# Kernel tuning notes

Hardware: AMD Instinct MI355X
Metric: run time of the kernel (lower is better)

Reference implementation:

```python
import jax, jax.numpy as jnp
import numpy as np
import math

B, IN_CH, IMG = 32, 3, 128
D, L, H, MLP, P = 512, 8, 8, 2048, 8
HD = D // H
EPS = 1e-5


def _conv(x, w, b, stride, pad):
    y = jax.lax.conv_general_dilated(x, w, (stride, stride), pad,
                                     dimension_numbers=("NCHW", "OIHW", "NCHW"))
    return y + b[None, :, None, None]


def _gn(x, g, b, groups):
    Bn, C, Hh, W = x.shape
    xr = x.reshape(Bn, groups, C // groups, Hh, W)
    m = jnp.mean(xr, axis=(2, 3, 4), keepdims=True)
    v = jnp.var(xr, axis=(2, 3, 4), keepdims=True)
    xr = (xr - m) / jnp.sqrt(v + EPS)
    return xr.reshape(Bn, C, Hh, W) * g[None, :, None, None] + b[None, :, None, None]


def _ln(x, g, b):
    m = jnp.mean(x, axis=-1, keepdims=True)
    v = jnp.var(x, axis=-1, keepdims=True)
    return (x - m) / jnp.sqrt(v + EPS) * g + b


def _rot_half(x):
    # interleaved pairs: (x0,x1) -> (-x1,x0)
    x1, x2 = x[..., 0::2], x[..., 1::2]
    return jnp.stack((-x2, x1), axis=-1).reshape(x.shape)


def _xpos_tables(n_pos, hd):
    # faithful to rotary_embedding_torch with use_xpos=True, scale_base=512
    inv = 1.0 / (10000.0 ** (jnp.arange(0, hd, 2, dtype=jnp.float32) / hd))
    seq = jnp.arange(n_pos, dtype=jnp.float32)
    freqs = jnp.repeat(seq[:, None] * inv[None, :], 2, axis=-1)  # (n_pos, hd) interleaved
    sv = (jnp.arange(0, hd, 2, dtype=jnp.float32) + 0.4 * hd) / (1.4 * hd)
    power = (seq - n_pos // 2) / 512.0
    scale = sv[None, :] ** power[:, None]                        # (n_pos, hd//2)
    scale = jnp.concatenate([scale, scale], axis=-1)             # library uses cat, not interleave
    return jnp.cos(freqs), jnp.sin(freqs), scale


def _pos2d(N, Dd):
    g = int(math.isqrt(N))
    y = jnp.tile(jnp.arange(g), g).astype(jnp.float32)
    x = jnp.repeat(jnp.arange(g), g).astype(jnp.float32)
    dq = Dd // 4
    omega = jnp.exp(jnp.arange(dq, dtype=jnp.float32) * -(math.log(10000.0) / dq))
    px, py = x[:, None] * omega, y[:, None] * omega
    return jnp.concatenate([jnp.sin(px), jnp.cos(px), jnp.sin(py), jnp.cos(py)], axis=-1)[None]


def setup_inputs() -> dict:
    key = jax.random.key(0)
    ks = iter(jax.random.split(key, 40))
    def rn(shape, s=0.02):
        return jax.random.normal(next(ks), shape, jnp.float32) * s
    return dict(
        x=jax.random.normal(next(ks), (B, IN_CH, IMG, IMG), jnp.float32),
        conv1_w=rn((32, 3, 3, 3)), conv1_b=jnp.zeros((32,), jnp.float32),
        gn1_g=jnp.ones((32,), jnp.float32), gn1_b=jnp.zeros((32,), jnp.float32),
        conv2_w=rn((64, 32, 3, 3)), conv2_b=jnp.zeros((64,), jnp.float32),
        gn2_g=jnp.ones((64,), jnp.float32), gn2_b=jnp.zeros((64,), jnp.float32),
        patch_w=rn((D, 64, P, P)), patch_b=jnp.zeros((D,), jnp.float32),
        cls_token=rn((1, 1, D), 1.0),
        ln1_g=jnp.ones((L, D), jnp.float32), ln1_b=jnp.zeros((L, D), jnp.float32),
        qkv_w=rn((L, D, 3 * D)), qkv_b=jnp.zeros((L, 3 * D), jnp.float32),
        out_w=rn((L, D, D)), out_b=jnp.zeros((L, D), jnp.float32),
        ln2_g=jnp.ones((L, D), jnp.float32), ln2_b=jnp.zeros((L, D), jnp.float32),
        w1_w=rn((L, D, MLP)), w1_b=jnp.zeros((L, MLP), jnp.float32),
        w2_w=rn((L, D, MLP)), w2_b=jnp.zeros((L, MLP), jnp.float32),
        w3_w=rn((L, MLP, D)), w3_b=jnp.zeros((L, D), jnp.float32),
        fn_g=jnp.ones((D,), jnp.float32), fn_b=jnp.zeros((D,), jnp.float32),
    )


def _forward(x, conv1_w, conv1_b, gn1_g, gn1_b, conv2_w, conv2_b, gn2_g, gn2_b,
             patch_w, patch_b, cls_token, ln1_g, ln1_b, qkv_w, qkv_b, out_w, out_b,
             ln2_g, ln2_b, w1_w, w1_b, w2_w, w2_b, w3_w, w3_b, fn_g, fn_b):
    # conv stem (no downsample)
    f = jax.nn.gelu(_gn(_conv(x, conv1_w, conv1_b, 1, [(1, 1), (1, 1)]), gn1_g, gn1_b, 4), approximate=False)
    f = jax.nn.gelu(_gn(_conv(f, conv2_w, conv2_b, 1, [(1, 1), (1, 1)]), gn2_g, gn2_b, 8), approximate=False)
    # patch embed
    p = _conv(f, patch_w, patch_b, P, "VALID")            # (B, D, g, g)
    Bn, Dd, gh, gw = p.shape
    tokens = p.reshape(Bn, Dd, gh * gw).transpose(0, 2, 1)  # (B, N, D)
    tokens = tokens + _pos2d(gh * gw, Dd)
    xa = jnp.concatenate([jnp.broadcast_to(cls_token, (Bn, 1, Dd)), tokens], axis=1)
    # NOTE: original code applies RoPE with seq_dim=-2 on (B,S,H,hd) -> rotation indexed by HEAD axis
    cos, sin, xsc = _xpos_tables(H, HD)
    scale_att = HD ** -0.5
    for i in range(L):
        n = _ln(xa, ln1_g[i], ln1_b[i])
        qkv = (n @ qkv_w[i] + qkv_b[i]).reshape(Bn, -1, 3, H, HD)
        q, k, v = qkv[:, :, 0], qkv[:, :, 1], qkv[:, :, 2]     # (B, S, H, hd)
        q = q * cos * xsc + _rot_half(q) * sin * xsc
        k = k * cos / xsc + _rot_half(k) * sin / xsc
        attn = jax.nn.softmax(jnp.einsum("bihd,bjhd->bhij", q, k) * scale_att, axis=-1)
        y = jnp.einsum("bhij,bjhd->bihd", attn, v).reshape(Bn, -1, Dd)
        xa = xa + y @ out_w[i] + out_b[i]
        n2 = _ln(xa, ln2_g[i], ln2_b[i])
        xa = xa + (jax.nn.silu(n2 @ w1_w[i] + w1_b[i]) * (n2 @ w2_w[i] + w2_b[i])) @ w3_w[i] + w3_b[i]
    return _ln(xa, fn_g, fn_b)


def reference(x, conv1_w, conv1_b, gn1_g, gn1_b, conv2_w, conv2_b, gn2_g, gn2_b,
              patch_w, patch_b, cls_token, ln1_g, ln1_b, qkv_w, qkv_b, out_w, out_b,
              ln2_g, ln2_b, w1_w, w1_b, w2_w, w2_b, w3_w, w3_b, fn_g, fn_b):
    xa = _forward(x, conv1_w, conv1_b, gn1_g, gn1_b, conv2_w, conv2_b, gn2_g, gn2_b,
                  patch_w, patch_b, cls_token, ln1_g, ln1_b, qkv_w, qkv_b, out_w, out_b,
                  ln2_g, ln2_b, w1_w, w1_b, w2_w, w2_b, w3_w, w3_b, fn_g, fn_b)
    return (xa[:, 0], xa[:, 1:])  # (cls, patches); grid_hw is static (16,16)
```

## Files before the change

### kernel.cpp

```cpp
#include <hip/hip_runtime.h>

#define EPSV 1e-5f
typedef unsigned short u16;
typedef short bf16x8 __attribute__((ext_vector_type(8)));
typedef float f32x4 __attribute__((ext_vector_type(4)));

__device__ __forceinline__ float gelu_exact(float x) {
    return 0.5f * x * (1.0f + erff(x * 0.7071067811865475f));
}
__device__ __forceinline__ u16 to_bf(float x) {
    union { float f; unsigned u; } c; c.f = x;
    unsigned r = c.u + 0x7fffu + ((c.u >> 16) & 1u);
    return (u16)(r >> 16);
}
__device__ __forceinline__ float to_f(u16 h) {
    union { unsigned u; float f; } c; c.u = ((unsigned)h) << 16;
    return c.f;
}
__device__ __forceinline__ void gload_lds16(const void* g, void* l) {
    __builtin_amdgcn_global_load_lds((const __attribute__((address_space(1))) unsigned int*)g,
                                     (__attribute__((address_space(3))) unsigned int*)l, 16, 0, 0);
}

__global__ void k_wsfail(float* out) { out[0] = 1.0e9f; }

__global__ void k_setup(float* __restrict__ sacc,
                        const float* __restrict__ conv1_w, float* __restrict__ w1t,
                        const float* __restrict__ conv2_w, u16* __restrict__ wpack,
                        const float* __restrict__ b1, const float* __restrict__ b2,
                        float* __restrict__ bias12,
                        float* __restrict__ postab, float* __restrict__ ropetab,
                        const float* __restrict__ cls, float* __restrict__ xa) {
    int idx = blockIdx.x * 256 + threadIdx.x;
    if (idx < 131072) {
        int p = idx >> 9, j = idx & 511;
        float coord = (j < 256) ? (float)(p >> 4) : (float)(p & 15);
        int jm = j & 127;
        float om = powf(10000.0f, -(float)jm / 128.0f);
        float arg = coord * om;
        postab[idx] = ((j >> 7) & 1) ? cosf(arg) : sinf(arg);
    }
    if (idx < 512) {
        int h = idx >> 6, d = idx & 63;
        float freq = (float)h * powf(10000.0f, -(float)(d >> 1) / 32.0f);
        float sv = (2.0f * (float)(d & 31) + 25.6f) / 89.6f;
        float pw = ((float)h - 4.0f) / 512.0f;
        float sc = powf(sv, pw);
        ropetab[idx * 4 + 0] = cosf(freq);
        ropetab[idx * 4 + 1] = sinf(freq);
        ropetab[idx * 4 + 2] = sc * 0.125f;
        ropetab[idx * 4 + 3] = 1.0f / sc;
    }
    if (idx < 768) sacc[idx] = 0.0f;
    if (idx < 864) {
        int co = idx / 27, k = idx % 27;
        w1t[k * 32 + co] = conv1_w[idx];
    }
    if (idx < 18432) {
        int ci = idx & 31, tc = idx >> 5;
        int tap = tc >> 6, co = tc & 63;
        wpack[idx] = to_bf(conv2_w[co * 288 + ci * 9 + tap]);
    }
    if (idx < 32768) {
        int l = idx >> 12, pc = idx & 4095;
        int chunk = pc >> 4, within = pc & 15;
        int srccol = (chunk >> 1) * 16 + within;
        bias12[idx] = (chunk & 1) ? b2[l * 2048 + srccol] : b1[l * 2048 + srccol];
    }
    if (idx < 16384) {
        int b = idx >> 9, d = idx & 511;
        xa[(size_t)(b * 257) * 512 + d] = cls[d];
    }
}

__global__ void k_pperm(const float* __restrict__ w, u16* __restrict__ wp) {
    int idx = blockIdx.x * 256 + threadIdx.x;
    int cout = idx >> 12, rem = idx & 4095;
    int tap = rem >> 6, ci = rem & 63;
    wp[idx] = to_bf(w[cout * 4096 + ci * 64 + tap]);
}

__global__ __launch_bounds__(256) void k_wcvtT(const float* __restrict__ src,
                                               u16* __restrict__ dst, int K, int N) {
    __shared__ float s[32][33];
    int z = blockIdx.z;
    src += (size_t)z * K * N;
    dst += (size_t)z * K * N;
    int k0 = blockIdx.y * 32, n0 = blockIdx.x * 32;
    int t = threadIdx.x, r = t >> 3, c4 = (t & 7) * 4;
    float4 v = *(const float4*)&src[(size_t)(k0 + r) * N + n0 + c4];
    s[r][c4 + 0] = v.x; s[r][c4 + 1] = v.y; s[r][c4 + 2] = v.z; s[r][c4 + 3] = v.w;
    __syncthreads();
    ushort4 o;
    o.x = to_bf(s[c4 + 0][r]); o.y = to_bf(s[c4 + 1][r]);
    o.z = to_bf(s[c4 + 2][r]); o.w = to_bf(s[c4 + 3][r]);
    *(ushort4*)&dst[(size_t)(n0 + r) * K + k0 + c4] = o;
}

__global__ __launch_bounds__(256) void k_wcvtT12L(const float* __restrict__ w1,
                                                  const float* __restrict__ w2,
                                                  u16* __restrict__ w12All) {
    __shared__ float s[32][33];
    int z = blockIdx.z;
    int layer = z >> 1, sel = z & 1;
    const float* src = (sel ? w2 : w1) + (size_t)layer * 1048576;
    u16* dst = w12All + (size_t)layer * 2097152;
    int k0 = blockIdx.y * 32, n0 = blockIdx.x * 32;
    int t = threadIdx.x, r = t >> 3, c4 = (t & 7) * 4;
    float4 v = *(const float4*)&src[(size_t)(k0 + r) * 2048 + n0 + c4];
    s[r][c4 + 0] = v.x; s[r][c4 + 1] = v.y; s[r][c4 + 2] = v.z; s[r][c4 + 3] = v.w;
    __syncthreads();
    ushort4 o;
    o.x = to_bf(s[c4 + 0][r]); o.y = to_bf(s[c4 + 1][r]);
    o.z = to_bf(s[c4 + 2][r]); o.w = to_bf(s[c4 + 3][r]);
    int nsrc = n0 + r;
    int p = ((nsrc >> 4) << 5) + (sel << 4) + (nsrc & 15);
    *(ushort4*)&dst[(size_t)p * 512 + k0 + c4] = o;
}

__global__ __launch_bounds__(256) void k_conv1(const float* __restrict__ in,
                                               const float* __restrict__ wt,
                                               const float* __restrict__ bias,
                                               u16* __restrict__ f1n,
                                               float* __restrict__ sacc) {
    __shared__ float s_in[3][18][18];
    __shared__ float rs[4][4], rq[4][4];
    int b = blockIdx.y;
    int tile = blockIdx.x;
    int y0 = (tile >> 3) << 4;
    int x0 = (tile & 7) << 4;
    int tid = threadIdx.x;
    for (int idx = tid; idx < 972; idx += 256) {
        int ci = idx / 324, r = idx % 324;
        int ly = r / 18, lx = r % 18;
        int gy = y0 + ly - 1, gx = x0 + lx - 1;
        float v = 0.0f;
        if (gy >= 0 && gy < 128 && gx >= 0 && gx < 128)
            v = in[((size_t)(b * 3 + ci) * 128 + gy) * 128 + gx];
        s_in[ci][ly][lx] = v;
    }
    __syncthreads();
    int py = tid >> 4, px = tid & 15;
    float acc[32];
#pragma unroll
    for (int co = 0; co < 32; co++) acc[co] = bias[co];
#pragma unroll
    for (int ci = 0; ci < 3; ci++)
#pragma unroll
        for (int dy = 0; dy < 3; dy++)
#pragma unroll
            for (int dx = 0; dx < 3; dx++) {
                float v = s_in[ci][py + dy][px + dx];
                const float* wr = &wt[(ci * 9 + dy * 3 + dx) * 32];
#pragma unroll
                for (int co = 0; co < 32; co++)
                    acc[co] = fmaf(wr[co], v, acc[co]);
            }
    float s[4] = {0.f, 0.f, 0.f, 0.f}, q[4] = {0.f, 0.f, 0.f, 0.f};
    u16 ob[32];
#pragma unroll
    for (int co = 0; co < 32; co++) {
        u16 hv = to_bf(acc[co]);
        ob[co] = hv;
        float v = to_f(hv);
        s[co >> 3] += v;
        q[co >> 3] += v * v;
    }
    int oy = y0 + py, ox = x0 + px;
    u16* dst = f1n + ((size_t)(b * 16384 + oy * 128 + ox) << 5);
#pragma unroll
    for (int i = 0; i < 8; i++)
        *(ushort4*)(dst + i * 4) = make_ushort4(ob[i * 4], ob[i * 4 + 1], ob[i * 4 + 2], ob[i * 4 + 3]);
#pragma unroll
    for (int g = 0; g < 4; g++) {
#pragma unroll
        for (int off = 1; off < 64; off <<= 1) {
            s[g] += __shfl_xor(s[g], off);
            q[g] += __shfl_xor(q[g], off);
        }
    }
    int w = tid >> 6, lane = tid & 63;
    if (lane == 0)
#pragma unroll
        for (int g = 0; g < 4; g++) { rs[g][w] = s[g]; rq[g][w] = q[g]; }
    __syncthreads();
    if (tid < 4) {
        int g = tid;
        float S = rs[g][0] + rs[g][1] + rs[g][2] + rs[g][3];
        float Q = rq[g][0] + rq[g][1] + rq[g][2] + rq[g][3];
        atomicAdd(&sacc[(b * 4 + g) * 2], S);
        atomicAdd(&sacc[(b * 4 + g) * 2 + 1], Q);
    }
}

__global__ void k_gnap(u16* __restrict__ xio, const float* __restrict__ sacc,
                       const float* __restrict__ gg, const float* __restrict__ bb,
                       int cm, int sh, int gmul) {
    int idx = blockIdx.x * 256 + threadIdx.x;
    long e = (long)idx * 4;
    int c0 = (int)(e & cm);
    int b = (int)(e >> sh);
    int sid = b * gmul + (c0 >> 3);
    float m = sacc[2 * sid] * (1.0f / 131072.0f);
    float var = sacc[2 * sid + 1] * (1.0f / 131072.0f) - m * m;
    float r = rsqrtf(var + 1e-5f);
    ushort4 a = *(ushort4*)&xio[e];
    ushort4 o;
    o.x = to_bf(gelu_exact((to_f(a.x) - m) * r * gg[c0 + 0] + bb[c0 + 0]));
    o.y = to_bf(gelu_exact((to_f(a.y) - m) * r * gg[c0 + 1] + bb[c0 + 1]));
    o.z = to_bf(gelu_exact((to_f(a.z) - m) * r * gg[c0 + 2] + bb[c0 + 2]));
    o.w = to_bf(gelu_exact((to_f(a.w) - m) * r * gg[c0 + 3] + bb[c0 + 3]));
    *(ushort4*)&xio[e] = o;
}

__global__ __launch_bounds__(256) void k_conv2m(const u16* __restrict__ f1b,
                                                const u16* __restrict__ wp,
                                                const float* __restrict__ bias,
                                                u16* __restrict__ f2n,
                                                float* __restrict__ sacc) {
    int b = blockIdx.y;
    int tile = blockIdx.x;
    int y0 = (tile >> 3) << 4;
    int x0 = (tile & 7) << 4;
    int tid = threadIdx.x;
    int w = tid >> 6, lane = tid & 63;
    int l15 = lane & 15, l16 = lane >> 4;

    const u16* base = f1b + ((size_t)b << 19);

    f32x4 acc[4][4];
    f32x4 zf = {0.f, 0.f, 0.f, 0.f};
#pragma unroll
    for (int m = 0; m < 4; m++)
#pragma unroll
        for (int n = 0; n < 4; n++) acc[m][n] = zf;
    bf16x8 zb = {0, 0, 0, 0, 0, 0, 0, 0};

#pragma unroll
    for (int tap = 0; tap < 9; tap++) {
        int dy = tap / 3, dx = tap % 3;
        int gx = x0 + l15 + dx - 1;
        bf16x8 af[4], bk[4];
#pragma unroll
        for (int m = 0; m < 4; m++) {
            int gy = y0 + w * 4 + m + dy - 1;
            bool ok = (gy >= 0) && (gy < 128) && (gx >= 0) && (gx < 128);
            int pix = ok ? (gy * 128 + gx) : 0;
            bf16x8 v = *(const bf16x8*)(base + ((size_t)pix << 5) + l16 * 8);
            af[m] = ok ? v : zb;
        }
#pragma unroll
        for (int n = 0; n < 4; n++)
            bk[n] = *(const bf16x8*)&wp[(tap * 64 + n * 16 + l15) * 32 + l16 * 8];
#pragma unroll
        for (int m = 0; m < 4; m++)
#pragma unroll
            for (int n = 0; n < 4; n++)
                acc[m][n] = __builtin_amdgcn_mfma_f32_16x16x32_bf16(af[m], bk[n], acc[m][n], 0, 0, 0);
    }

#pragma unroll
    for (int n = 0; n < 4; n++) {
        int gco = n * 16 + l15;
        float bv = bias[gco];
        float sn = 0.0f, qn = 0.0f;
#pragma unroll
        for (int m = 0; m < 4; m++) {
            int py = w * 4 + m;
#pragma unroll
            for (int r = 0; r < 4; r++) {
                int px = l16 * 4 + r;
                float v = acc[m][n][r] + bv;
                u16 hv = to_bf(v);
                f2n[((size_t)(b * 16384 + (y0 + py) * 128 + x0 + px) << 6) + gco] = hv;
                float vf = to_f(hv);
                sn += vf;
                qn += vf * vf;
            }
        }
#pragma unroll
        for (int off = 1; off <= 4; off <<= 1) { sn += __shfl_xor(sn, off); qn += __shfl_xor(qn, off); }
        sn += __shfl_xor(sn, 16); qn += __shfl_xor(qn, 16);
        sn += __shfl_xor(sn, 32); qn += __shfl_xor(qn, 32);
        if (lane == 0 || lane == 8) {
            int g = n * 2 + (lane >> 3);
            atomicAdd(&sacc[(b * 8 + g) * 2], sn);
            atomicAdd(&sacc[(b * 8 + g) * 2 + 1], qn);
        }
    }
}

template <int MODE, int EPI>
__global__ __launch_bounds__(256) void k_bgemm(const u16* __restrict__ A,
                                               const u16* __restrict__ Bt,
                                               const float* __restrict__ bias,
                                               void* __restrict__ Cp,
                                               const float* __restrict__ aux,
                                               int M, int N, int K) {
    __shared__ u16 ldsA[8192];
    __shared__ u16 ldsB[8192];
    int tid = threadIdx.x;
    int w = tid >> 6, lane = tid & 63;
    int bm = blockIdx.y * 128, bn = blockIdx.x * 128;
    int wr = w >> 1, wc = w & 1;
    int l15 = lane & 15, l16 = lane >> 4;

    f32x4 acc[4][4];
    f32x4 zf = {0.f, 0.f, 0.f, 0.f};
#pragma unroll
    for (int m = 0; m < 4; m++)
#pragma unroll
        for (int n = 0; n < 4; n++) acc[m][n] = zf;

    for (int k0 = 0; k0 < K; k0 += 64) {
#pragma unroll
        for (int i = 0; i < 4; i++) {
            int chunk = (w * 4 + i) * 64 + lane;
            int kg = chunk >> 7, row = chunk & 127;
            const u16* src;
            if (MODE == 0) {
                int grow = bm + row;
                if (grow > M - 1) grow = M - 1;
                src = A + (size_t)grow * K + k0 + kg * 8;
            } else {
                int grow = bm + row;
                int bimg = grow >> 8, p = grow & 255;
                int kga = (k0 >> 3) + kg;
                int tap = kga >> 3, cq = kga & 7;
                int ky = tap >> 3, kx = tap & 7;
                int gy = ((p >> 4) << 3) + ky, gx = ((p & 15) << 3) + kx;
                src = A + (((size_t)(bimg * 16384 + gy * 128 + gx)) << 6) + cq * 8;
            }
            gload_lds16(src, &ldsA[(w * 4 + i) * 512]);
        }
#pragma unroll
        for (int i = 0; i < 4; i++) {
            int chunk = (w * 4 + i) * 64 + lane;
            int col = chunk >> 3, kgs = chunk & 7;
            int kg_src = kgs ^ (col & 7);
            const u16* src = Bt + (size_t)(bn + col) * K + k0 + kg_src * 8;
            gload_lds16(src, &ldsB[(w * 4 + i) * 512]);
        }
        __syncthreads();

        bf16x8 af[4][2], bfr[4][2];
#pragma unroll
        for (int kk = 0; kk < 2; kk++) {
            int kga = kk * 4 + l16;
#pragma unroll
            for (int m = 0; m < 4; m++) {
                int row_l = wr * 64 + m * 16 + l15;
                af[m][kk] = *(const bf16x8*)&ldsA[(kga * 128 + row_l) * 8];
            }
#pragma unroll
            for (int n = 0; n < 4; n++) {
                int col_l = wc * 64 + n * 16 + l15;
                bfr[n][kk] = *(const bf16x8*)&ldsB[(col_l * 8 + (kga ^ (col_l & 7))) * 8];
            }
        }
#pragma unroll
        for (int m = 0; m < 4; m++)
#pragma unroll
            for (int n = 0; n < 4; n++) {
                acc[m][n] = __builtin_amdgcn_mfma_f32_16x16x32_bf16(af[m][0], bfr[n][0], acc[m][n], 0, 0, 0);
                acc[m][n] = __builtin_amdgcn_mfma_f32_16x16x32_bf16(af[m][1], bfr[n][1], acc[m][n], 0, 0, 0);
            }
        __syncthreads();
    }

    if (EPI == 6) {
#pragma unroll
        for (int np = 0; np < 2; np++) {
            int n_a = np * 2, n_b = np * 2 + 1;
            float bva = bias[bn + wc * 64 + n_a * 16 + l15];
            float bvb = bias[bn + wc * 64 + n_b * 16 + l15];
            int ocol = (bn >> 1) + wc * 32 + np * 16 + l15;
#pragma unroll
            for (int m = 0; m < 4; m++) {
#pragma unroll
                for (int r = 0; r < 4; r++) {
                    int grow = bm + wr * 64 + m * 16 + l16 * 4 + r;
                    if (grow < M) {
                        float h1v = to_f(to_bf(acc[m][n_a][r] + bva));
                        float h2v = to_f(to_bf(acc[m][n_b][r] + bvb));
                        float sl = h1v / (1.0f + __expf(-h1v));
                        ((u16*)Cp)[(size_t)grow * (N >> 1) + ocol] = to_bf(sl * h2v);
                    }
                }
            }
        }
    } else {
#pragma unroll
        for (int n = 0; n < 4; n++) {
            int gcol = bn + wc * 64 + n * 16 + l15;
            float bv = bias[gcol];
            float rc = 0.f, rsn = 0.f, rsc = 1.f;
            bool isqk = false, odd = false;
            if (EPI == 7) {
                isqk = gcol < 1024;
                odd = (l15 & 1) != 0;
                const float* rb = &aux[(gcol & 511) * 4];
                if (isqk) {
                    rc = rb[0]; rsn = rb[1];
                    rsc = (gcol < 512) ? rb[2] : rb[3];
                }
            }
#pragma unroll
            for (int m = 0; m < 4; m++) {
#pragma unroll
                for (int r = 0; r < 4; r++) {
                    int grow = bm + wr * 64 + m * 16 + l16 * 4 + r;
                    float v = acc[m][n][r] + bv;
                    if (EPI == 7) {
                        float p = __shfl_xor(v, 1);
                        float vr = isqk ? ((odd ? (v * rc + p * rsn) : (v * rc - p * rsn)) * rsc) : v;
                        if (grow < M) ((u16*)Cp)[(size_t)grow * N + gcol] = to_bf(vr);
                    } else if (EPI == 1) {
                        if (grow < M) ((float*)Cp)[(size_t)grow * N + gcol] = v;
                    } else if (EPI == 2) {
                        if (grow < M) ((float*)Cp)[(size_t)grow * N + gcol] += v;
                    } else {
                        int bimg = grow >> 8, p2 = grow & 255;
                        v += aux[p2 * 512 + gcol];
                        ((float*)Cp)[((size_t)(bimg * 257) + 1 + p2) * 512 + gcol] = v;
                    }
                }
            }
        }
    }
}

__global__ __launch_bounds__(256) void k_lnb(const float* __restrict__ x,
                                             const float* __restrict__ g,
                                             const float* __restrict__ bta,
                                             u16* __restrict__ o) {
    int row = blockIdx.x * 4 + (threadIdx.x >> 6);
    int lane = threadIdx.x & 63;
    const float4* xr = (const float4*)(x + (size_t)row * 512);
    float4 a = xr[lane * 2], b = xr[lane * 2 + 1];
    float s = a.x + a.y + a.z + a.w + b.x + b.y + b.z + b.w;
#pragma unroll
    for (int off = 1; off < 64; off <<= 1) s += __shfl_xor(s, off);
    float mean = s * (1.0f / 512.0f);
    float d[8] = {a.x - mean, a.y - mean, a.z - mean, a.w - mean,
                  b.x - mean, b.y - mean, b.z - mean, b.w - mean};
    float q = 0.0f;
#pragma unroll
    for (int i = 0; i < 8; i++) q += d[i] * d[i];
#pragma unroll
    for (int off = 1; off < 64; off <<= 1) q += __shfl_xor(q, off);
    float rstd = rsqrtf(q * (1.0f / 512.0f) + EPSV);
    int c0 = lane * 8;
    float4 g0 = *(const float4*)&g[c0], g1 = *(const float4*)&g[c0 + 4];
    float4 b0 = *(const float4*)&bta[c0], b1 = *(const float4*)&bta[c0 + 4];
    u16* orow = o + (size_t)row * 512 + c0;
    *(ushort4*)orow = make_ushort4(to_bf(d[0] * rstd * g0.x + b0.x), to_bf(d[1] * rstd * g0.y + b0.y),
                                   to_bf(d[2] * rstd * g0.z + b0.z), to_bf(d[3] * rstd * g0.w + b0.w));
    *(ushort4*)(orow + 4) = make_ushort4(to_bf(d[4] * rstd * g1.x + b1.x), to_bf(d[5] * rstd * g1.y + b1.y),
                                         to_bf(d[6] * rstd * g1.z + b1.z), to_bf(d[7] * rstd * g1.w + b1.w));
}

__global__ __launch_bounds__(256) void k_ln_out(const float* __restrict__ x,
                                                const float* __restrict__ g,
                                                const float* __restrict__ bta,
                                                float* __restrict__ out) {
    int row = blockIdx.x * 4 + (threadIdx.x >> 6);
    int lane = threadIdx.x & 63;
    const float4* xr = (const float4*)(x + (size_t)row * 512);
    float4 a = xr[lane * 2], b = xr[lane * 2 + 1];
    float s = a.x + a.y + a.z + a.w + b.x + b.y + b.z + b.w;
#pragma unroll
    for (int off = 1; off < 64; off <<= 1) s += __shfl_xor(s, off);
    float mean = s * (1.0f / 512.0f);
    float d[8] = {a.x - mean, a.y - mean, a.z - mean, a.w - mean,
                  b.x - mean, b.y - mean, b.z - mean, b.w - mean};
    float q = 0.0f;
#pragma unroll
    for (int i = 0; i < 8; i++) q += d[i] * d[i];
#pragma unroll
    for (int off = 1; off < 64; off <<= 1) q += __shfl_xor(q, off);
    float rstd = rsqrtf(q * (1.0f / 512.0f) + EPSV);
    int bb = row / 257, t = row % 257;
    float* dst = (t == 0) ? out + (size_t)bb * 512
                          : out + 16384 + (size_t)(bb * 256 + (t - 1)) * 512;
    int c0 = lane * 8;
    float4 g0 = *(const float4*)&g[c0], g1 = *(const float4*)&g[c0 + 4];
    float4 b0 = *(const float4*)&bta[c0], b1 = *(const float4*)&bta[c0 + 4];
    *(float4*)(dst + c0) = make_float4(d[0] * rstd * g0.x + b0.x, d[1] * rstd * g0.y + b0.y,
                                       d[2] * rstd * g0.z + b0.z, d[3] * rstd * g0.w + b0.w);
    *(float4*)(dst + c0 + 4) = make_float4(d[4] * rstd * g1.x + b1.x, d[5] * rstd * g1.y + b1.y,
                                           d[6] * rstd * g1.z + b1.z, d[7] * rstd * g1.w + b1.w);
}

__global__ __launch_bounds__(256) void k_attn_mfma(const u16* __restrict__ qkv,
                                                   u16* __restrict__ y) {
    __shared__ u16 KV[2][64][72];
    __shared__ float sc[32][260];
    __shared__ u16 Pb[32][328];
    __shared__ float red1[32][8];
    __shared__ float red2[32][8];
    __shared__ float invr[32];

    int bid = blockIdx.x;
    int qt = bid % 9, bh = bid / 9;
    int h = bh & 7, b = bh >> 3;
    int q0 = qt * 32;
    int tid = threadIdx.x;
    int w = tid >> 6, lane = tid & 63;
    int l15 = lane & 15, l16 = lane >> 4;

    bf16x8 aq[2][2];
#pragma unroll
    for (int m = 0; m < 2; m++) {
        int grow = q0 + m * 16 + l15; if (grow > 256) grow = 256;
        const u16* qp = qkv + (size_t)(b * 257 + grow) * 1536 + h * 64 + l16 * 8;
        aq[m][0] = *(const bf16x8*)qp;
        aq[m][1] = *(const bf16x8*)(qp + 32);
    }

    for (int t = 0; t < 5; t++) {
        int j0 = t * 64;
        int gk = j0 + w * 16 + l15; if (gk > 256) gk = 256;
        const u16* kp = qkv + (size_t)(b * 257 + gk) * 1536 + 512 + h * 64 + l16 * 8;
        bf16x8 bk0 = *(const bf16x8*)kp;
        bf16x8 bk1 = *(const bf16x8*)(kp + 32);
        f32x4 a2[2];
        f32x4 zf = {0.f, 0.f, 0.f, 0.f};
#pragma unroll
        for (int m = 0; m < 2; m++) {
            a2[m] = zf;
            a2[m] = __builtin_amdgcn_mfma_f32_16x16x32_bf16(aq[m][0], bk0, a2[m], 0, 0, 0);
            a2[m] = __builtin_amdgcn_mfma_f32_16x16x32_bf16(aq[m][1], bk1, a2[m], 0, 0, 0);
        }
        int col = j0 + w * 16 + l15;
        if (col < 257) {
#pragma unroll
            for (int m = 0; m < 2; m++)
#pragma unroll
                for (int r = 0; r < 4; r++)
                    sc[m * 16 + l16 * 4 + r][col] = a2[m][r];
        }
    }
    __syncthreads();

    {
        int r = tid >> 3, sub = tid & 7;
        float mx = -1e30f;
        for (int j = sub; j < 257; j += 8) mx = fmaxf(mx, sc[r][j]);
        red1[r][sub] = mx;
        __syncthreads();
        mx = red1[r][0];
#pragma unroll
        for (int i = 1; i < 8; i++) mx = fmaxf(mx, red1[r][i]);
        float sm = 0.0f;
        for (int j = sub; j < 257; j += 8) {
            float e = __expf(sc[r][j] - mx);
            Pb[r][j] = to_bf(e);
            sm += e;
        }
        for (int j = 257 + sub; j < 320; j += 8) Pb[r][j] = 0;
        red2[r][sub] = sm;
        __syncthreads();
        if (sub == 0) {
            float t = red2[r][0];
#pragma unroll
            for (int i = 1; i < 8; i++) t += red2[r][i];
            invr[r] = 1.0f / t;
        }
        __syncthreads();
    }

    f32x4 oacc[2];
    {
        f32x4 zf = {0.f, 0.f, 0.f, 0.f};
        oacc[0] = zf; oacc[1] = zf;
    }
    for (int t = 0; t < 5; t++) {
        int j0 = t * 64;
        int buf = t & 1;
        {
            int vk = tid & 63, vd0 = (tid >> 6) * 16;
            int gk = j0 + vk;
            u16 o[16];
            if (gk <= 256) {
                const u16* vp = qkv + (size_t)(b * 257 + gk) * 1536 + 1024 + h * 64 + vd0;
                ushort4 a0 = *(const ushort4*)vp, a1 = *(const ushort4*)(vp + 4);
                ushort4 a2v = *(const ushort4*)(vp + 8), a3 = *(const ushort4*)(vp + 12);
                o[0] = a0.x; o[1] = a0.y; o[2] = a0.z; o[3] = a0.w;
                o[4] = a1.x; o[5] = a1.y; o[6] = a1.z; o[7] = a1.w;
                o[8] = a2v.x; o[9] = a2v.y; o[10] = a2v.z; o[11] = a2v.w;
                o[12] = a3.x; o[13] = a3.y; o[14] = a3.z; o[15] = a3.w;
            } else {
#pragma unroll
                for (int i = 0; i < 16; i++) o[i] = 0;
            }
#pragma unroll
            for (int i = 0; i < 16; i++) KV[buf][vd0 + i][vk] = o[i];
        }
        __syncthreads();

        bf16x8 ap[2][2], bv[2];
#pragma unroll
        for (int m = 0; m < 2; m++)
#pragma unroll
            for (int kk = 0; kk < 2; kk++)
                ap[m][kk] = *(const bf16x8*)&Pb[m * 16 + l15][j0 + kk * 32 + l16 * 8];
#pragma unroll
        for (int kk = 0; kk < 2; kk++)
            bv[kk] = *(const bf16x8*)&KV[buf][w * 16 + l15][kk * 32 + l16 * 8];
#pragma unroll
        for (int m = 0; m < 2; m++) {
            oacc[m] = __builtin_amdgcn_mfma_f32_16x16x32_bf16(ap[m][0], bv[0], oacc[m], 0, 0, 0);
            oacc[m] = __builtin_amdgcn_mfma_f32_16x16x32_bf16(ap[m][1], bv[1], oacc[m], 0, 0, 0);
        }
    }

#pragma unroll
    for (int m = 0; m < 2; m++)
#pragma unroll
        for (int r = 0; r < 4; r++) {
            int lr = m * 16 + l16 * 4 + r;
            int grow = q0 + lr;
            if (grow < 257)
                y[(size_t)(b * 257 + grow) * 512 + h * 64 + w * 16 + l15] =
                    to_bf(oacc[m][r] * invr[lr]);
        }
}

extern "C" void kernel_launch(void* const* d_in, const int* in_sizes, int n_in,
                              void* d_out, int out_size, void* d_ws, size_t ws_size,
                              hipStream_t stream) {
    const float* x       = (const float*)d_in[0];
    const float* conv1_w = (const float*)d_in[1];
    const float* conv1_b = (const float*)d_in[2];
    const float* gn1_g   = (const float*)d_in[3];
    const float* gn1_b   = (const float*)d_in[4];
    const float* conv2_w = (const float*)d_in[5];
    const float* conv2_b = (const float*)d_in[6];
    const float* gn2_g   = (const float*)d_in[7];
    const float* gn2_b   = (const float*)d_in[8];
    const float* patch_w = (const float*)d_in[9];
    const float* patch_b = (const float*)d_in[10];
    const float* cls_tok = (const float*)d_in[11];
    const float* ln1_g   = (const float*)d_in[12];
    const float* ln1_b   = (const float*)d_in[13];
    const float* qkv_w   = (const float*)d_in[14];
    const float* qkv_b   = (const float*)d_in[15];
    const float* out_w   = (const float*)d_in[16];
    const float* out_b   = (const float*)d_in[17];
    const float* ln2_g   = (const float*)d_in[18];
    const float* ln2_b   = (const float*)d_in[19];
    const float* w1_w    = (const float*)d_in[20];
    const float* w1_b    = (const float*)d_in[21];
    const float* w2_w    = (const float*)d_in[22];
    const float* w2_b    = (const float*)d_in[23];
    const float* w3_w    = (const float*)d_in[24];
    const float* w3_b    = (const float*)d_in[25];
    const float* fn_g    = (const float*)d_in[26];
    const float* fn_b    = (const float*)d_in[27];
    float* out = (float*)d_out;
    char* wsb  = (char*)d_ws;

    const size_t O_R1    = 0;
    const size_t O_W12A  = 0;
    const size_t O_W3A   = 33554432;
    const size_t O_HB    = O_R1 + 67371008;
    const size_t O_NB    = O_R1 + 101056512;
    const size_t O_Y     = O_R1 + 109477888;
    const size_t O_R2    = 134217728;
    const size_t O_XA    = 201326592;
    const size_t O_PWT   = 218169344;
    const size_t O_QKVT  = 222363648;
    const size_t O_OUTT  = 234946560;
    const size_t O_PT    = 245432320;
    const size_t O_RT    = 245956608;
    const size_t O_CW1   = 245964800;
    const size_t O_CW2   = 245968896;
    const size_t O_SA    = 246046720;
    const size_t O_B12   = 246050816;
    const size_t NEED    = 246181888;
    if (ws_size < NEED) {
        k_wsfail<<<1, 1, 0, stream>>>(out);
        return;
    }
    u16*   f2n    = (u16*)(wsb + O_R1);
    u16*   w12All = (u16*)(wsb + O_W12A);
    u16*   w3All  = (u16*)(wsb + O_W3A);
    u16*   hb     = (u16*)(wsb + O_HB);
    u16*   nb     = (u16*)(wsb + O_NB);
    u16*   yb     = (u16*)(wsb + O_Y);
    u16*   f1n    = (u16*)(wsb + O_R2);
    u16*   qkvb   = (u16*)(wsb + O_R2);
    float* xa     = (float*)(wsb + O_XA);
    u16*   patchT = (u16*)(wsb + O_PWT);
    u16*   qkvT   = (u16*)(wsb + O_QKVT);
    u16*   outT   = (u16*)(wsb + O_OUTT);
    float* postab = (float*)(wsb + O_PT);
    float* ropet  = (float*)(wsb + O_RT);
    float* w1t    = (float*)(wsb + O_CW1);
    u16*   wpack  = (u16*)(wsb + O_CW2);
    float* sacc   = (float*)(wsb + O_SA);
    float* bias12 = (float*)(wsb + O_B12);

    k_setup<<<512, 256, 0, stream>>>(sacc, conv1_w, w1t, conv2_w, wpack,
                                     w1_b, w2_b, bias12, postab, ropet, cls_tok, xa);
    k_pperm<<<8192, 256, 0, stream>>>(patch_w, patchT);
    k_wcvtT<<<dim3(48, 16, 8), 256, 0, stream>>>(qkv_w, qkvT, 512, 1536);
    k_wcvtT<<<dim3(16, 16, 8), 256, 0, stream>>>(out_w, outT, 512, 512);

    k_conv1<<<dim3(64, 32), 256, 0, stream>>>(x, w1t, conv1_b, f1n, sacc);
    k_gnap<<<16384, 256, 0, stream>>>(f1n, sacc, gn1_g, gn1_b, 31, 19, 4);
    k_conv2m<<<dim3(64, 32), 256, 0, stream>>>(f1n, wpack, conv2_b, f2n, sacc + 256);
    k_gnap<<<32768, 256, 0, stream>>>(f2n, sacc + 256, gn2_g, gn2_b, 63, 20, 8);

    k_bgemm<1, 3><<<dim3(4, 64), 256, 0, stream>>>(f2n, patchT, patch_b, xa, postab, 8192, 512, 4096);

    k_wcvtT12L<<<dim3(64, 16, 16), 256, 0, stream>>>(w1_w, w2_w, w12All);
    k_wcvtT<<<dim3(16, 64, 8), 256, 0, stream>>>(w3_w, w3All, 2048, 512);

    for (int l = 0; l < 8; l++) {
        k_lnb<<<2056, 256, 0, stream>>>(xa, ln1_g + l * 512, ln1_b + l * 512, nb);
        k_bgemm<0, 7><<<dim3(12, 65), 256, 0, stream>>>(nb, qkvT + (size_t)l * 786432,
                                                        qkv_b + l * 1536, qkvb, ropet, 8224, 1536, 512);
        k_attn_mfma<<<2304, 256, 0, stream>>>(qkvb, yb);
        k_bgemm<0, 2><<<dim3(4, 65), 256, 0, stream>>>(yb, outT + (size_t)l * 262144,
                                                       out_b + l * 512, xa, nullptr, 8224, 512, 512);
        k_lnb<<<2056, 256, 0, stream>>>(xa, ln2_g + l * 512, ln2_b + l * 512, nb);
        k_bgemm<0, 6><<<dim3(32, 65), 256, 0, stream>>>(nb, w12All + (size_t)l * 2097152,
                                                        bias12 + l * 4096, hb, nullptr, 8224, 4096, 512);
        k_bgemm<0, 2><<<dim3(4, 65), 256, 0, stream>>>(hb, w3All + (size_t)l * 1048576,
                                                       w3_b + l * 512, xa, nullptr, 8224, 512, 2048);
    }
    k_ln_out<<<2056, 256, 0, stream>>>(xa, fn_g, fn_b, out);
}
```

Measured before the change: 2.556 ms.

## Add 64-row GEMM for N=512 projections, stage conv2 stores via LDS, prioritize MFMA

Adds a k_bgemm64 kernel with 64x128 tiles for the out-projection and w3 GEMMs, roughly doubling the block count from 260 to 516 so more CUs are busy on the N=512 residual GEMMs. The conv2 epilogue now stages results in LDS and writes each pixel's 64 channels as contiguous 16-byte vectors. Its group-norm statistics are reduced per block before the atomics, cutting atomic traffic. Attention MFMA sections get s_setprio hints. The trade-offs are extra LDS and barriers in conv2 and less reuse per tile in the smaller GEMM.

```diff
diff --git a/kernel.cpp b/kernel.cpp
--- a/kernel.cpp
+++ b/kernel.cpp
@@ -4,6 +4,7 @@
 typedef unsigned short u16;
 typedef short bf16x8 __attribute__((ext_vector_type(8)));
 typedef float f32x4 __attribute__((ext_vector_type(4)));
+typedef u16 u16x8 __attribute__((ext_vector_type(8)));
 
 __device__ __forceinline__ float gelu_exact(float x) {
     return 0.5f * x * (1.0f + erff(x * 0.7071067811865475f));
@@ -218,6 +219,8 @@
                                                 const float* __restrict__ bias,
                                                 u16* __restrict__ f2n,
                                                 float* __restrict__ sacc) {
+    __shared__ u16 st[256][72];
+    __shared__ float rs[8][4], rq[8][4];
     int b = blockIdx.y;
     int tile = blockIdx.x;
     int y0 = (tile >> 3) << 4;
@@ -261,32 +264,53 @@
 
 #pragma unroll
     for (int n = 0; n < 4; n++) {
-        int gco = n * 16 + l15;
-        float bv = bias[gco];
-        float sn = 0.0f, qn = 0.0f;
+        int ch = n * 16 + l15;
+        float bv = bias[ch];
 #pragma unroll
         for (int m = 0; m < 4; m++) {
-            int py = w * 4 + m;
 #pragma unroll
             for (int r = 0; r < 4; r++) {
-                int px = l16 * 4 + r;
-                float v = acc[m][n][r] + bv;
-                u16 hv = to_bf(v);
-                f2n[((size_t)(b * 16384 + (y0 + py) * 128 + x0 + px) << 6) + gco] = hv;
-                float vf = to_f(hv);
-                sn += vf;
-                qn += vf * vf;
-            }
-        }
-#pragma unroll
-        for (int off = 1; off <= 4; off <<= 1) { sn += __shfl_xor(sn, off); qn += __shfl_xor(qn, off); }
-        sn += __shfl_xor(sn, 16); qn += __shfl_xor(qn, 16);
-        sn += __shfl_xor(sn, 32); qn += __shfl_xor(qn, 32);
-        if (lane == 0 || lane == 8) {
-            int g = n * 2 + (lane >> 3);
-            atomicAdd(&sacc[(b * 8 + g) * 2], sn);
-            atomicAdd(&sacc[(b * 8 + g) * 2 + 1], qn);
-        }
+                int lpix = (w * 4 + m) * 16 + l16 * 4 + r;
+                st[lpix][ch] = to_bf(acc[m][n][r] + bv);
+            }
+        }
+    }
+    __syncthreads();
+
+    int py = tid >> 4, pxx = tid & 15;
+    u16* dstp = f2n + ((size_t)(b * 16384 + (y0 + py) * 128 + x0 + pxx) << 6);
+    float gs[8], gq[8];
+#pragma unroll
+    for (int g = 0; g < 8; g++) { gs[g] = 0.0f; gq[g] = 0.0f; }
+#pragma unroll
+    for (int c0 = 0; c0 < 8; c0++) {
+        u16x8 v = *(const u16x8*)&st[tid][c0 * 8];
+        *(u16x8*)(dstp + c0 * 8) = v;
+#pragma unroll
+        for (int i = 0; i < 8; i++) {
+            float f = to_f((u16)v[i]);
+            gs[c0] += f;
+            gq[c0] += f * f;
+        }
+    }
+#pragma unroll
+    for (int g = 0; g < 8; g++) {
+#pragma unroll
+        for (int off = 1; off < 64; off <<= 1) {
+            gs[g] += __shfl_xor(gs[g], off);
+            gq[g] += __shfl_xor(gq[g], off);
+        }
+    }
+    if (lane == 0)
+#pragma unroll
+        for (int g = 0; g < 8; g++) { rs[g][w] = gs[g]; rq[g][w] = gq[g]; }
+    __syncthreads();
+    if (tid < 8) {
+        int g = tid;
+        float S = rs[g][0] + rs[g][1] + rs[g][2] + rs[g][3];
+        float Q = rq[g][0] + rq[g][1] + rq[g][2] + rq[g][3];
+        atomicAdd(&sacc[(b * 8 + g) * 2], S);
+        atomicAdd(&sacc[(b * 8 + g) * 2 + 1], Q);
     }
 }
 
@@ -430,6 +454,85 @@
     }
 }
 
+__global__ __launch_bounds__(256) void k_bgemm64(const u16* __restrict__ A,
+                                                 const u16* __restrict__ Bt,
+                                                 const float* __restrict__ bias,
+                                                 float* __restrict__ C,
+                                                 int M, int N, int K) {
+    __shared__ u16 ldsA[4096];
+    __shared__ u16 ldsB[8192];
+    int tid = threadIdx.x;
+    int w = tid >> 6, lane = tid & 63;
+    int bm = blockIdx.y * 64, bn = blockIdx.x * 128;
+    int l15 = lane & 15, l16 = lane >> 4;
+
+    f32x4 acc[4][2];
+    f32x4 zf = {0.f, 0.f, 0.f, 0.f};
+#pragma unroll
+    for (int m = 0; m < 4; m++)
+#pragma unroll
+        for (int n = 0; n < 2; n++) acc[m][n] = zf;
+
+    for (int k0 = 0; k0 < K; k0 += 64) {
+#pragma unroll
+        for (int i = 0; i < 2; i++) {
+            int chunk = (w * 2 + i) * 64 + lane;
+            int kg = chunk >> 6, row = chunk & 63;
+            int grow = bm + row;
+            if (grow > M - 1) grow = M - 1;
+            const u16* src = A + (size_t)grow * K + k0 + kg * 8;
+            gload_lds16(src, &ldsA[(w * 2 + i) * 512]);
+        }
+#pragma unroll
+        for (int i = 0; i < 4; i++) {
+            int chunk = (w * 4 + i) * 64 + lane;
+            int col = chunk >> 3, kgs = chunk & 7;
+            int kg_src = kgs ^ (col & 7);
+            const u16* src = Bt + (size_t)(bn + col) * K + k0 + kg_src * 8;
+            gload_lds16(src, &ldsB[(w * 4 + i) * 512]);
+        }
+        __syncthreads();
+
+        bf16x8 af[4][2], bfr[2][2];
+#pragma unroll
+        for (int kk = 0; kk < 2; kk++) {
+            int kga = kk * 4 + l16;
+#pragma unroll
+            for (int m = 0; m < 4; m++) {
+                int row_l = m * 16 + l15;
+                af[m][kk] = *(const bf16x8*)&ldsA[(kga * 64 + row_l) * 8];
+            }
+#pragma unroll
+            for (int n = 0; n < 2; n++) {
+                int col_l = w * 32 + n * 16 + l15;
+                bfr[n][kk] = *(const bf16x8*)&ldsB[(col_l * 8 + (kga ^ (col_l & 7))) * 8];
+            }
+        }
+#pragma unroll
+        for (int m = 0; m < 4; m++)
+#pragma unroll
+            for (int n = 0; n < 2; n++) {
+                acc[m][n] = __builtin_amdgcn_mfma_f32_16x16x32_bf16(af[m][0], bfr[n][0], acc[m][n], 0, 0, 0);
+                acc[m][n] = __builtin_amdgcn_mfma_f32_16x16x32_bf16(af[m][1], bfr[n][1], acc[m][n], 0, 0, 0);
+            }
+        __syncthreads();
+    }
+
+#pragma unroll
+    for (int n = 0; n < 2; n++) {
+        int gcol = bn + w * 32 + n * 16 + l15;
+        float bv = bias[gcol];
+#pragma unroll
+        for (int m = 0; m < 4; m++) {
+#pragma unroll
+            for (int r = 0; r < 4; r++) {
+                int grow = bm + m * 16 + l16 * 4 + r;
+                if (grow < M) C[(size_t)grow * N + gcol] += acc[m][n][r] + bv;
+            }
+        }
+    }
+}
+
 __global__ __launch_bounds__(256) void k_lnb(const float* __restrict__ x,
                                              const float* __restrict__ g,
                                              const float* __restrict__ bta,
@@ -526,12 +629,14 @@
         bf16x8 bk1 = *(const bf16x8*)(kp + 32);
         f32x4 a2[2];
         f32x4 zf = {0.f, 0.f, 0.f, 0.f};
+        __builtin_amdgcn_s_setprio(1);
 #pragma unroll
         for (int m = 0; m < 2; m++) {
             a2[m] = zf;
             a2[m] = __builtin_amdgcn_mfma_f32_16x16x32_bf16(aq[m][0], bk0, a2[m], 0, 0, 0);
             a2[m] = __builtin_amdgcn_mfma_f32_16x16x32_bf16(aq[m][1], bk1, a2[m], 0, 0, 0);
         }
+        __builtin_amdgcn_s_setprio(0);
         int col = j0 + w * 16 + l15;
         if (col < 257) {
 #pragma unroll
@@ -608,11 +713,13 @@
 #pragma unroll
         for (int kk = 0; kk < 2; kk++)
             bv[kk] = *(const bf16x8*)&KV[buf][w * 16 + l15][kk * 32 + l16 * 8];
+        __builtin_amdgcn_s_setprio(1);
 #pragma unroll
         for (int m = 0; m < 2; m++) {
             oacc[m] = __builtin_amdgcn_mfma_f32_16x16x32_bf16(ap[m][0], bv[0], oacc[m], 0, 0, 0);
             oacc[m] = __builtin_amdgcn_mfma_f32_16x16x32_bf16(ap[m][1], bv[1], oacc[m], 0, 0, 0);
         }
+        __builtin_amdgcn_s_setprio(0);
     }
 
 #pragma unroll
@@ -723,13 +830,13 @@
         k_bgemm<0, 7><<<dim3(12, 65), 256, 0, stream>>>(nb, qkvT + (size_t)l * 786432,
                                                         qkv_b + l * 1536, qkvb, ropet, 8224, 1536, 512);
         k_attn_mfma<<<2304, 256, 0, stream>>>(qkvb, yb);
-        k_bgemm<0, 2><<<dim3(4, 65), 256, 0, stream>>>(yb, outT + (size_t)l * 262144,
-                                                       out_b + l * 512, xa, nullptr, 8224, 512, 512);
+        k_bgemm64<<<dim3(4, 129), 256, 0, stream>>>(yb, outT + (size_t)l * 262144,
+                                                    out_b + l * 512, xa, 8224, 512, 512);
         k_lnb<<<2056, 256, 0, stream>>>(xa, ln2_g + l * 512, ln2_b + l * 512, nb);
         k_bgemm<0, 6><<<dim3(32, 65), 256, 0, stream>>>(nb, w12All + (size_t)l * 2097152,
                                                         bias12 + l * 4096, hb, nullptr, 8224, 4096, 512);
-        k_bgemm<0, 2><<<dim3(4, 65), 256, 0, stream>>>(hb, w3All + (size_t)l * 1048576,
-                                                       w3_b + l * 512, xa, nullptr, 8224, 512, 2048);
+        k_bgemm64<<<dim3(4, 129), 256, 0, stream>>>(hb, w3All + (size_t)l * 1048576,
+                                                    w3_b + l * 512, xa, 8224, 512, 2048);
     }
     k_ln_out<<<2056, 256, 0, stream>>>(xa, fn_g, fn_b, out);
 }
```

Measured after the change: 2.269 ms, median of 2. 1.13x faster.
